# Kernel optimization log

Hardware: AMD Instinct MI355X
Metric: run time of the kernel (lower is better)

Reference implementation:

```python
import jax, jax.numpy as jnp
import numpy as np

N = 50000   # nodes
E = 512000  # edges
D = 64      # embedding_dim
L = 4       # num_layers
ATOM_DIMS = np.array([119, 5, 12, 12, 10, 6, 6, 2, 2])  # OGB atom feature vocab sizes
BOND_DIMS = np.array([5, 6, 2])                          # OGB bond feature vocab sizes


def _ln(x, g, b, eps=1e-5):
    m = x.mean(-1, keepdims=True)
    v = x.var(-1, keepdims=True)
    return (x - m) * jax.lax.rsqrt(v + eps) * g + b


def setup_inputs() -> dict:
    key = jax.random.key(0)
    ks = jax.random.split(key, 12)
    s = 0.05
    x = jax.random.randint(ks[0], (N, 9), 0, jnp.asarray(ATOM_DIMS)[None, :])
    edge_attr = jax.random.randint(ks[1], (E, 3), 0, jnp.asarray(BOND_DIMS)[None, :])
    edge_index = jax.random.randint(ks[2], (2, E), 0, N)
    # padded embedding tables: [n_feats, max_vocab, D]
    atom_emb = jax.random.normal(ks[3], (9, 119, D), jnp.float32) * s
    bond_emb = jax.random.normal(ks[4], (3, 6, D), jnp.float32) * s
    eps = jnp.zeros((L,), jnp.float32)  # GIN eps, init 0
    W1 = jax.random.normal(ks[5], (L, D, 2 * D), jnp.float32) * s
    b1 = jnp.zeros((L, 2 * D), jnp.float32)
    W2 = jax.random.normal(ks[6], (L, 2 * D, D), jnp.float32) * s
    b2 = jnp.zeros((L, D), jnp.float32)
    ln_g = jnp.ones((L, D), jnp.float32)
    ln_b = jnp.zeros((L, D), jnp.float32)
    Wu1 = jax.random.normal(ks[7], (L, 3 * D, 3 * D), jnp.float32) * s
    bu1 = jnp.zeros((L, 3 * D), jnp.float32)
    ug = jnp.ones((L, 3 * D), jnp.float32)
    ub = jnp.zeros((L, 3 * D), jnp.float32)
    Wu2 = jax.random.normal(ks[8], (L, 3 * D, D), jnp.float32) * s
    bu2 = jnp.zeros((L, D), jnp.float32)
    return dict(x=x, edge_attr=edge_attr, edge_index=edge_index,
                atom_emb=atom_emb, bond_emb=bond_emb, eps=eps,
                W1=W1, b1=b1, W2=W2, b2=b2, ln_g=ln_g, ln_b=ln_b,
                Wu1=Wu1, bu1=bu1, ug=ug, ub=ub, Wu2=Wu2, bu2=bu2)


def reference(x, edge_attr, edge_index, atom_emb, bond_emb, eps,
              W1, b1, W2, b2, ln_g, ln_b, Wu1, bu1, ug, ub, Wu2, bu2):
    # Atom/Bond encoders: sum of per-column categorical embeddings
    node = atom_emb[jnp.arange(9)[None, :], x].sum(axis=1)       # [N, D]
    edge = bond_emb[jnp.arange(3)[None, :], edge_attr].sum(axis=1)  # [E, D]
    src, dst = edge_index[0], edge_index[1]
    for l in range(L):
        # MyGINConv (GINE): aggregate relu(x_src + e) at dst, mlp((1+eps)x + agg)
        msg = jax.nn.relu(node[src] + edge)                      # [E, D]
        agg = jax.ops.segment_sum(msg, dst, num_segments=N)      # [N, D]
        h = (1.0 + eps[l]) * node + agg
        h = jax.nn.relu(h @ W1[l] + b1[l]) @ W2[l] + b2[l]       # conv MLP
        h = _ln(h, ln_g[l], ln_b[l])                             # batch_norms[l] (LayerNorm)
        node = jax.nn.relu(h) + node                             # dropout=identity (eval) + residual
        # SparseEdgeUpdateLayer (residual=True)
        cat = jnp.concatenate([node[src], node[dst], edge], axis=-1)  # [E, 3D]
        m = _ln(cat @ Wu1[l] + bu1[l], ug[l], ub[l])
        edge = jax.nn.relu(m) @ Wu2[l] + bu2[l] + edge
    return node, edge
```

## Files before the change

### kernel.cpp

```cpp
#include <hip/hip_runtime.h>
#include <hip/hip_bf16.h>


#define GIN_N 50000
#define GIN_E 512000

typedef __attribute__((ext_vector_type(8))) short short8;
typedef __attribute__((ext_vector_type(4))) float f32x4;
typedef unsigned short u16;

__device__ __forceinline__ u16 bf16r(float x) {
    unsigned u = __builtin_bit_cast(unsigned, x);
    u += 0x7fffu + ((u >> 16) & 1u);
    return (u16)(u >> 16);
}
__device__ __forceinline__ float bf16f(u16 h) {
    unsigned u = ((unsigned)h) << 16;
    return __builtin_bit_cast(float, u);
}

__global__ __launch_bounds__(256) void zero_f32(float* __restrict__ p, int n) {
    int i = blockIdx.x * 256 + threadIdx.x;
    if (i < n) p[i] = 0.f;
}

__global__ __launch_bounds__(256) void atom_encode(const int* __restrict__ x,
        const float* __restrict__ emb, float* __restrict__ node, int N) {
    int idx = blockIdx.x * 256 + threadIdx.x;
    int n = idx >> 6, lane = idx & 63;
    if (n >= N) return;
    float s = 0.f;
#pragma unroll
    for (int f = 0; f < 9; ++f) {
        int v = x[n * 9 + f];
        s += emb[(f * 119 + v) * 64 + lane];
    }
    node[(size_t)n * 64 + lane] = s;
}

__global__ __launch_bounds__(256) void bond_encode_scatter(
        const int* __restrict__ ea, const float* __restrict__ emb,
        u16* __restrict__ edgeB, const int* __restrict__ src,
        const int* __restrict__ dst, const float* __restrict__ node,
        float* __restrict__ agg, int E) {
    int idx = blockIdx.x * 256 + threadIdx.x;
    int e = idx >> 6, lane = idx & 63;
    if (e >= E) return;
    float s = 0.f;
#pragma unroll
    for (int f = 0; f < 3; ++f) {
        int v = ea[e * 3 + f];
        s += emb[(f * 6 + v) * 64 + lane];
    }
    edgeB[(size_t)e * 64 + lane] = bf16r(s);
    int si = src[e], di = dst[e];
    float msg = fmaxf(node[(size_t)si * 64 + lane] + s, 0.f);
    unsafeAtomicAdd(&agg[(size_t)di * 64 + lane], msg);
}

__global__ __launch_bounds__(256) void pack_b1(const float* __restrict__ W,
        u16* __restrict__ out, int K, int Nc, int F) {
    int tid = blockIdx.x * 256 + threadIdx.x;
    int lane = tid & 63;
    int frag = (tid >> 6) % F;
    int layer = tid / (F * 64);
    int tpr = Nc / 16;
    int ks = frag / tpr, tt = frag % tpr;
    int k0 = ks * 32 + ((lane >> 4) << 3);
    int col = tt * 16 + (lane & 15);
    const float* w = W + (size_t)layer * K * Nc;
    u16* o = out + ((size_t)layer * F + frag) * 512 + (size_t)lane * 8;
#pragma unroll
    for (int j = 0; j < 8; ++j) o[j] = bf16r(w[(size_t)(k0 + j) * Nc + col]);
}
__global__ __launch_bounds__(256) void pack_b2(const float* __restrict__ W,
        u16* __restrict__ out, int K, int Nc, int F) {
    int tid = blockIdx.x * 256 + threadIdx.x;
    int lane = tid & 63;
    int frag = (tid >> 6) % F;
    int layer = tid / (F * 64);
    int tpr = Nc / 16;
    int ks = frag / tpr, tt = frag % tpr;
    int k0 = ks * 32 + ((lane >> 4) << 3);
    int col = tt * 16 + (lane & 15);
    const float* w = W + (size_t)layer * K * Nc;
    u16* o = out + ((size_t)layer * F + frag) * 1024 + (size_t)lane * 8;
#pragma unroll
    for (int j = 0; j < 8; ++j) {
        float v = w[(size_t)(k0 + j) * Nc + col];
        u16 hi = bf16r(v);
        o[j] = hi;
        o[512 + j] = bf16r(v - bf16f(hi));
    }
}

__global__ __launch_bounds__(256, 2) void node_mlp(
        float* __restrict__ node, u16* __restrict__ nodeB,
        float* __restrict__ agg,
        const float* __restrict__ epsArr, int l,
        const u16* __restrict__ pw1, const u16* __restrict__ pw2,
        const float* __restrict__ b1, const float* __restrict__ b2,
        const float* __restrict__ lng, const float* __restrict__ lnb, int N) {
    __shared__ u16 xH[64][72], xL[64][72];
    __shared__ u16 hH[64][136], hL[64][136];
    __shared__ float pS[4][64], pS2[4][64], lnM[64], lnR[64];
    const int t = threadIdx.x, w = t >> 6, lane = t & 63;
    const int g = lane >> 4, c0 = lane & 15;
    const float epf = 1.f + epsArr[l];

#pragma unroll
    for (int i = 0; i < 16; ++i) {
        int r = w * 16 + i;
        int n = blockIdx.x * 64 + r;
        float x = 0.f;
        if (n < N) {
            size_t o = (size_t)n * 64 + lane;
            x = epf * node[o] + agg[o];
            agg[o] = 0.f;
        }
        u16 h = bf16r(x);
        xH[r][lane] = h;
        xL[r][lane] = bf16r(x - bf16f(h));
    }
    __syncthreads();

    f32x4 a1[4][2];
#pragma unroll
    for (int sp = 0; sp < 4; ++sp)
#pragma unroll
        for (int lt = 0; lt < 2; ++lt) a1[sp][lt] = (f32x4)0.f;
#pragma unroll
    for (int ks = 0; ks < 2; ++ks) {
        short8 aH[4], aL[4];
#pragma unroll
        for (int sp = 0; sp < 4; ++sp) {
            aH[sp] = *(const short8*)&xH[sp * 16 + c0][ks * 32 + g * 8];
            aL[sp] = *(const short8*)&xL[sp * 16 + c0][ks * 32 + g * 8];
        }
#pragma unroll
        for (int lt = 0; lt < 2; ++lt) {
            const u16* p = pw1 + (size_t)(ks * 8 + w * 2 + lt) * 1024 + (size_t)lane * 8;
            short8 bH = *(const short8*)p;
            short8 bL = *(const short8*)(p + 512);
#pragma unroll
            for (int sp = 0; sp < 4; ++sp) {
                a1[sp][lt] = __builtin_amdgcn_mfma_f32_16x16x32_bf16(aH[sp], bH, a1[sp][lt], 0, 0, 0);
                a1[sp][lt] = __builtin_amdgcn_mfma_f32_16x16x32_bf16(aH[sp], bL, a1[sp][lt], 0, 0, 0);
                a1[sp][lt] = __builtin_amdgcn_mfma_f32_16x16x32_bf16(aL[sp], bH, a1[sp][lt], 0, 0, 0);
            }
        }
    }
#pragma unroll
    for (int lt = 0; lt < 2; ++lt) {
        int col = w * 32 + lt * 16 + c0;
        float bias = b1[col];
#pragma unroll
        for (int sp = 0; sp < 4; ++sp)
#pragma unroll
            for (int rg = 0; rg < 4; ++rg) {
                int r = sp * 16 + g * 4 + rg;
                float v = fmaxf(a1[sp][lt][rg] + bias, 0.f);
                u16 h = bf16r(v);
                hH[r][col] = h;
                hL[r][col] = bf16r(v - bf16f(h));
            }
    }
    __syncthreads();

    f32x4 a2[4];
#pragma unroll
    for (int sp = 0; sp < 4; ++sp) a2[sp] = (f32x4)0.f;
#pragma unroll
    for (int ks = 0; ks < 4; ++ks) {
        const u16* p = pw2 + (size_t)(ks * 4 + w) * 1024 + (size_t)lane * 8;
        short8 bH = *(const short8*)p;
        short8 bL = *(const short8*)(p + 512);
#pragma unroll
        for (int sp = 0; sp < 4; ++sp) {
            short8 aH = *(const short8*)&hH[sp * 16 + c0][ks * 32 + g * 8];
            short8 aL = *(const short8*)&hL[sp * 16 + c0][ks * 32 + g * 8];
            a2[sp] = __builtin_amdgcn_mfma_f32_16x16x32_bf16(aH, bH, a2[sp], 0, 0, 0);
            a2[sp] = __builtin_amdgcn_mfma_f32_16x16x32_bf16(aH, bL, a2[sp], 0, 0, 0);
            a2[sp] = __builtin_amdgcn_mfma_f32_16x16x32_bf16(aL, bH, a2[sp], 0, 0, 0);
        }
    }
    float bias2 = b2[w * 16 + c0];
    float s1v[4][4], s2v[4][4];
#pragma unroll
    for (int sp = 0; sp < 4; ++sp)
#pragma unroll
        for (int rg = 0; rg < 4; ++rg) {
            float v = a2[sp][rg] + bias2;
            a2[sp][rg] = v;
            s1v[sp][rg] = v;
            s2v[sp][rg] = v * v;
        }
#pragma unroll
    for (int off = 1; off < 16; off <<= 1)
#pragma unroll
        for (int sp = 0; sp < 4; ++sp)
#pragma unroll
            for (int rg = 0; rg < 4; ++rg) {
                s1v[sp][rg] += __shfl_xor(s1v[sp][rg], off);
                s2v[sp][rg] += __shfl_xor(s2v[sp][rg], off);
            }
    if (c0 == 0) {
#pragma unroll
        for (int sp = 0; sp < 4; ++sp)
#pragma unroll
            for (int rg = 0; rg < 4; ++rg) {
                int r = sp * 16 + g * 4 + rg;
                pS[w][r] = s1v[sp][rg];
                pS2[w][r] = s2v[sp][rg];
            }
    }
    __syncthreads();
    if (t < 64) {
        float a = pS[0][t] + pS[1][t] + pS[2][t] + pS[3][t];
        float b = pS2[0][t] + pS2[1][t] + pS2[2][t] + pS2[3][t];
        float mean = a * (1.f / 64.f);
        float var = b * (1.f / 64.f) - mean * mean;
        lnM[t] = mean;
        lnR[t] = rsqrtf(var + 1e-5f);
    }
    __syncthreads();

    int col = w * 16 + c0;
    float gg = lng[col], bc = lnb[col];
#pragma unroll
    for (int sp = 0; sp < 4; ++sp)
#pragma unroll
        for (int rg = 0; rg < 4; ++rg) {
            int r = sp * 16 + g * 4 + rg;
            int n = blockIdx.x * 64 + r;
            if (n < N) {
                size_t o = (size_t)n * 64 + col;
                float y = (a2[sp][rg] - lnM[r]) * lnR[r] * gg + bc;
                float out = fmaxf(y, 0.f) + node[o];
                node[o] = out;
                nodeB[o] = bf16r(out);
            }
        }
}

template <bool SCATTER>
__global__ __launch_bounds__(256, 4) void edge_update_v6(
        const int* __restrict__ src, const int* __restrict__ dst,
        const float* __restrict__ node, const u16* __restrict__ nodeB,
        u16* __restrict__ edgeB, float* __restrict__ edgeF,
        float* __restrict__ agg,
        const u16* __restrict__ pb1, const u16* __restrict__ pb2,
        const float* __restrict__ bu1, const float* __restrict__ ug,
        const float* __restrict__ ub, const float* __restrict__ bu2) {
    __shared__ u16 cat[64][202];
    __shared__ u16 eold[64][66];
    __shared__ float pS[4][64], pS2[4][64];
    __shared__ float lnM[64], lnR[64];
    const int t = threadIdx.x, w = t >> 6, lane = t & 63;
    const int g = lane >> 4, c0 = lane & 15;
    const long eB = (long)blockIdx.x * 64;

#pragma unroll
    for (int i = 0; i < 16; ++i) {
        int r = w * 16 + i;
        long ge = eB + r;
        int s = src[ge], d = dst[ge];
        cat[r][lane]       = nodeB[(size_t)s * 64 + lane];
        cat[r][64 + lane]  = nodeB[(size_t)d * 64 + lane];
        u16 ev = edgeB[(size_t)ge * 64 + lane];
        cat[r][128 + lane] = ev;
        eold[r][lane] = ev;
    }
    __syncthreads();

    f32x4 acc[4][3];
#pragma unroll
    for (int sp = 0; sp < 4; ++sp)
#pragma unroll
        for (int lt = 0; lt < 3; ++lt) acc[sp][lt] = (f32x4)0.f;
#pragma unroll
    for (int ks = 0; ks < 6; ++ks) {
        short8 a[4];
#pragma unroll
        for (int sp = 0; sp < 4; ++sp)
            a[sp] = *(const short8*)&cat[sp * 16 + c0][ks * 32 + g * 8];
#pragma unroll
        for (int lt = 0; lt < 3; ++lt) {
            const u16* p = pb1 + (size_t)(ks * 12 + w * 3 + lt) * 512 + (size_t)lane * 8;
            short8 b = *(const short8*)p;
#pragma unroll
            for (int sp = 0; sp < 4; ++sp)
                acc[sp][lt] = __builtin_amdgcn_mfma_f32_16x16x32_bf16(a[sp], b, acc[sp][lt], 0, 0, 0);
        }
    }

    float bs[3];
#pragma unroll
    for (int lt = 0; lt < 3; ++lt) bs[lt] = bu1[w * 48 + lt * 16 + c0];
    float s1v[4][4], s2v[4][4];
#pragma unroll
    for (int sp = 0; sp < 4; ++sp)
#pragma unroll
        for (int rg = 0; rg < 4; ++rg) { s1v[sp][rg] = 0.f; s2v[sp][rg] = 0.f; }
#pragma unroll
    for (int sp = 0; sp < 4; ++sp)
#pragma unroll
        for (int lt = 0; lt < 3; ++lt)
#pragma unroll
            for (int rg = 0; rg < 4; ++rg) {
                float v = acc[sp][lt][rg] + bs[lt];
                acc[sp][lt][rg] = v;
                s1v[sp][rg] += v;
                s2v[sp][rg] += v * v;
            }
#pragma unroll
    for (int off = 1; off < 16; off <<= 1)
#pragma unroll
        for (int sp = 0; sp < 4; ++sp)
#pragma unroll
            for (int rg = 0; rg < 4; ++rg) {
                s1v[sp][rg] += __shfl_xor(s1v[sp][rg], off);
                s2v[sp][rg] += __shfl_xor(s2v[sp][rg], off);
            }
    if (c0 == 0) {
#pragma unroll
        for (int sp = 0; sp < 4; ++sp)
#pragma unroll
            for (int rg = 0; rg < 4; ++rg) {
                int r = sp * 16 + g * 4 + rg;
                pS[w][r] = s1v[sp][rg];
                pS2[w][r] = s2v[sp][rg];
            }
    }
    __syncthreads();
    if (t < 64) {
        float a = pS[0][t] + pS[1][t] + pS[2][t] + pS[3][t];
        float b = pS2[0][t] + pS2[1][t] + pS2[2][t] + pS2[3][t];
        float mean = a * (1.f / 192.f);
        float var = b * (1.f / 192.f) - mean * mean;
        lnM[t] = mean;
        lnR[t] = rsqrtf(var + 1e-5f);
    }
    __syncthreads();

#pragma unroll
    for (int lt = 0; lt < 3; ++lt) {
        int col = w * 48 + lt * 16 + c0;
        float gg = ug[col], bb = ub[col];
#pragma unroll
        for (int sp = 0; sp < 4; ++sp)
#pragma unroll
            for (int rg = 0; rg < 4; ++rg) {
                int r = sp * 16 + g * 4 + rg;
                float v = (acc[sp][lt][rg] - lnM[r]) * lnR[r] * gg + bb;
                cat[r][col] = bf16r(fmaxf(v, 0.f));
            }
    }
    __syncthreads();

    f32x4 a2[4];
#pragma unroll
    for (int sp = 0; sp < 4; ++sp) a2[sp] = (f32x4)0.f;
#pragma unroll
    for (int ks = 0; ks < 6; ++ks) {
        const u16* p = pb2 + (size_t)(ks * 4 + w) * 512 + (size_t)lane * 8;
        short8 b = *(const short8*)p;
#pragma unroll
        for (int sp = 0; sp < 4; ++sp) {
            short8 a = *(const short8*)&cat[sp * 16 + c0][ks * 32 + g * 8];
            a2[sp] = __builtin_amdgcn_mfma_f32_16x16x32_bf16(a, b, a2[sp], 0, 0, 0);
        }
    }

    const int col = w * 16 + c0;
    const float bb2 = bu2[col];
#pragma unroll
    for (int sp = 0; sp < 4; ++sp)
#pragma unroll
        for (int rg = 0; rg < 4; ++rg) {
            int r = sp * 16 + g * 4 + rg;
            long ge = eB + r;
            float eNew = a2[sp][rg] + bb2 + bf16f(eold[r][col]);
            if (SCATTER) {
                edgeB[(size_t)ge * 64 + col] = bf16r(eNew);
                int s2 = src[ge], d2 = dst[ge];
                float msg = fmaxf(node[(size_t)s2 * 64 + col] + eNew, 0.f);
                unsafeAtomicAdd(&agg[(size_t)d2 * 64 + col], msg);
            } else {
                edgeF[(size_t)ge * 64 + col] = eNew;
            }
        }
}

extern "C" void kernel_launch(void* const* d_in, const int* in_sizes, int n_in,
                              void* d_out, int out_size, void* d_ws, size_t ws_size,
                              hipStream_t stream) {
    const int*   x         = (const int*)d_in[0];
    const int*   edge_attr = (const int*)d_in[1];
    const int*   edge_index= (const int*)d_in[2];
    const float* atom_emb  = (const float*)d_in[3];
    const float* bond_emb  = (const float*)d_in[4];
    const float* eps       = (const float*)d_in[5];
    const float* W1        = (const float*)d_in[6];
    const float* b1        = (const float*)d_in[7];
    const float* W2        = (const float*)d_in[8];
    const float* b2        = (const float*)d_in[9];
    const float* ln_g      = (const float*)d_in[10];
    const float* ln_b      = (const float*)d_in[11];
    const float* Wu1       = (const float*)d_in[12];
    const float* bu1       = (const float*)d_in[13];
    const float* ug        = (const float*)d_in[14];
    const float* ub        = (const float*)d_in[15];
    const float* Wu2       = (const float*)d_in[16];
    const float* bu2       = (const float*)d_in[17];

    const int N = GIN_N, E = GIN_E;
    const int* src = edge_index;
    const int* dst = edge_index + E;

    float* node  = (float*)d_out;
    float* edgeF = (float*)d_out + (size_t)N * 64;

    char* ws = (char*)d_ws;
    float* agg   = (float*)ws;  ws += (size_t)N * 64 * 4;
    u16*   nodeB = (u16*)ws;    ws += (size_t)N * 64 * 2;
    u16*   edgeB = (u16*)ws;    ws += (size_t)E * 64 * 2;
    u16* pb1     = (u16*)ws;    ws += (size_t)4 * 72 * 512 * 2;
    u16* pb2     = (u16*)ws;    ws += (size_t)4 * 24 * 512 * 2;
    u16* pw1     = (u16*)ws;    ws += (size_t)4 * 16 * 1024 * 2;
    u16* pw2     = (u16*)ws;    ws += (size_t)4 * 16 * 1024 * 2;

    pack_b1<<<(4 * 72 * 64) / 256, 256, 0, stream>>>(Wu1, pb1, 192, 192, 72);
    pack_b1<<<(4 * 24 * 64) / 256, 256, 0, stream>>>(Wu2, pb2, 192, 64, 24);
    pack_b2<<<(4 * 16 * 64) / 256, 256, 0, stream>>>(W1, pw1, 64, 128, 16);
    pack_b2<<<(4 * 16 * 64) / 256, 256, 0, stream>>>(W2, pw2, 128, 64, 16);

    atom_encode<<<(N * 64 + 255) / 256, 256, 0, stream>>>(x, atom_emb, node, N);
    zero_f32<<<(N * 64) / 256, 256, 0, stream>>>(agg, N * 64);
    bond_encode_scatter<<<(E * 64) / 256, 256, 0, stream>>>(edge_attr, bond_emb,
        edgeB, src, dst, node, agg, E);

    const int nodeBlocks = (N + 63) / 64;
    for (int l = 0; l < 4; ++l) {
        node_mlp<<<nodeBlocks, 256, 0, stream>>>(node, nodeB, agg, eps, l,
            pw1 + (size_t)l * 16 * 1024, pw2 + (size_t)l * 16 * 1024,
            b1 + (size_t)l * 128, b2 + (size_t)l * 64,
            ln_g + (size_t)l * 64, ln_b + (size_t)l * 64, N);
        if (l < 3)
            edge_update_v6<true><<<E / 64, 256, 0, stream>>>(src, dst, node, nodeB,
                edgeB, edgeF, agg,
                pb1 + (size_t)l * 72 * 512, pb2 + (size_t)l * 24 * 512,
                bu1 + (size_t)l * 192,
                ug + (size_t)l * 192, ub + (size_t)l * 192,
                bu2 + (size_t)l * 64);
        else
            edge_update_v6<false><<<E / 64, 256, 0, stream>>>(src, dst, node, nodeB,
                edgeB, edgeF, agg,
                pb1 + (size_t)l * 72 * 512, pb2 + (size_t)l * 24 * 512,
                bu1 + (size_t)l * 192,
                ug + (size_t)l * 192, ub + (size_t)l * 192,
                bu2 + (size_t)l * 64);
    }
}
```

Before: 912.7 us.

## Sort edges by destination via CSR and pre-reduce scatter atomics in shared memory

Builds a destination-sorted edge permutation each call (histogram, single-block scan, atomic fill) and processes edges in sorted order. Edge messages are staged in shared memory and summed over runs of equal destination, so one atomic is issued per run instead of per edge. The final edge output is written back through the permutation. Block indices are also remapped with an 8-way interleave to spread tiles. This adds several preprocessing kernels, including a serial single-block scan, and makes the final edge writes scattered.

```diff
diff --git a/kernel.cpp b/kernel.cpp
--- a/kernel.cpp
+++ b/kernel.cpp
@@ -22,6 +22,10 @@
 __global__ __launch_bounds__(256) void zero_f32(float* __restrict__ p, int n) {
     int i = blockIdx.x * 256 + threadIdx.x;
     if (i < n) p[i] = 0.f;
+}
+__global__ __launch_bounds__(256) void zero_i32(int* __restrict__ p, int n) {
+    int i = blockIdx.x * 256 + threadIdx.x;
+    if (i < n) p[i] = 0;
 }
 
 __global__ __launch_bounds__(256) void atom_encode(const int* __restrict__ x,
@@ -38,22 +42,73 @@
     node[(size_t)n * 64 + lane] = s;
 }
 
+__global__ __launch_bounds__(256) void csr_hist(const int* __restrict__ dst,
+                                                int* __restrict__ deg, int E) {
+    int e = blockIdx.x * 256 + threadIdx.x;
+    if (e < E) atomicAdd(&deg[dst[e]], 1);
+}
+__global__ __launch_bounds__(256) void csr_scan(const int* __restrict__ deg,
+                                                int* __restrict__ cursor, int N) {
+    __shared__ int ps[256];
+    const int t = threadIdx.x;
+    const int chunk = (N + 255) / 256;
+    const int base = t * chunk;
+    int s = 0;
+    for (int i = 0; i < chunk; ++i) {
+        int idx = base + i;
+        if (idx < N) s += deg[idx];
+    }
+    ps[t] = s;
+    __syncthreads();
+    for (int off = 1; off < 256; off <<= 1) {
+        int v = (t >= off) ? ps[t - off] : 0;
+        __syncthreads();
+        ps[t] += v;
+        __syncthreads();
+    }
+    int run = ps[t] - s;
+    for (int i = 0; i < chunk; ++i) {
+        int idx = base + i;
+        if (idx < N) { cursor[idx] = run; run += deg[idx]; }
+    }
+}
+__global__ __launch_bounds__(256) void csr_fill(const int* __restrict__ dst,
+        int* __restrict__ cursor, int* __restrict__ perm, int E) {
+    int e = blockIdx.x * 256 + threadIdx.x;
+    if (e < E) {
+        int d = dst[e];
+        int pos = atomicAdd(&cursor[d], 1);
+        perm[pos] = e;
+    }
+}
+__global__ __launch_bounds__(256) void permute_ei(const int* __restrict__ src,
+        const int* __restrict__ dst, const int* __restrict__ perm,
+        int* __restrict__ srcS, int* __restrict__ dstS, int E) {
+    int i = blockIdx.x * 256 + threadIdx.x;
+    if (i < E) {
+        int pe = perm[i];
+        srcS[i] = src[pe];
+        dstS[i] = dst[pe];
+    }
+}
+
 __global__ __launch_bounds__(256) void bond_encode_scatter(
         const int* __restrict__ ea, const float* __restrict__ emb,
-        u16* __restrict__ edgeB, const int* __restrict__ src,
-        const int* __restrict__ dst, const float* __restrict__ node,
-        float* __restrict__ agg, int E) {
+        u16* __restrict__ edgeB, const int* __restrict__ perm,
+        const int* __restrict__ srcS, const int* __restrict__ dstS,
+        const float* __restrict__ node, float* __restrict__ agg, int E) {
     int idx = blockIdx.x * 256 + threadIdx.x;
     int e = idx >> 6, lane = idx & 63;
     if (e >= E) return;
+    int pe = perm[e];
     float s = 0.f;
 #pragma unroll
     for (int f = 0; f < 3; ++f) {
-        int v = ea[e * 3 + f];
+        int v = ea[pe * 3 + f];
         s += emb[(f * 6 + v) * 64 + lane];
     }
     edgeB[(size_t)e * 64 + lane] = bf16r(s);
-    int si = src[e], di = dst[e];
+    int si = srcS[e], di = dstS[e];
     float msg = fmaxf(node[(size_t)si * 64 + lane] + s, 0.f);
     unsafeAtomicAdd(&agg[(size_t)di * 64 + lane], msg);
 }
@@ -244,8 +299,9 @@
 }
 
 template <bool SCATTER>
-__global__ __launch_bounds__(256, 4) void edge_update_v6(
+__global__ __launch_bounds__(256, 4) void edge_update_v7(
         const int* __restrict__ src, const int* __restrict__ dst,
+        const int* __restrict__ perm,
         const float* __restrict__ node, const u16* __restrict__ nodeB,
         u16* __restrict__ edgeB, float* __restrict__ edgeF,
         float* __restrict__ agg,
@@ -256,10 +312,13 @@
     __shared__ u16 eold[64][66];
     __shared__ float pS[4][64], pS2[4][64];
     __shared__ float lnM[64], lnR[64];
+    __shared__ int dstL[64], srcL[64];
     const int t = threadIdx.x, w = t >> 6, lane = t & 63;
     const int g = lane >> 4, c0 = lane & 15;
-    const long eB = (long)blockIdx.x * 64;
-
+    const int tile = (blockIdx.x & 7) * (gridDim.x >> 3) + (blockIdx.x >> 3);
+    const long eB = (long)tile * 64;
+
+    if (t < 64) { dstL[t] = dst[eB + t]; srcL[t] = src[eB + t]; }
 #pragma unroll
     for (int i = 0; i < 16; ++i) {
         int r = w * 16 + i;
@@ -371,7 +430,9 @@
             a2[sp] = __builtin_amdgcn_mfma_f32_16x16x32_bf16(a, b, a2[sp], 0, 0, 0);
         }
     }
-
+    __syncthreads();
+
+    float* msgF = (float*)&cat[0][0];
     const int col = w * 16 + c0;
     const float bb2 = bu2[col];
 #pragma unroll
@@ -383,13 +444,28 @@
             float eNew = a2[sp][rg] + bb2 + bf16f(eold[r][col]);
             if (SCATTER) {
                 edgeB[(size_t)ge * 64 + col] = bf16r(eNew);
-                int s2 = src[ge], d2 = dst[ge];
-                float msg = fmaxf(node[(size_t)s2 * 64 + col] + eNew, 0.f);
-                unsafeAtomicAdd(&agg[(size_t)d2 * 64 + col], msg);
+                float msg = fmaxf(node[(size_t)srcL[r] * 64 + col] + eNew, 0.f);
+                msgF[r * 66 + col] = msg;
             } else {
-                edgeF[(size_t)ge * 64 + col] = eNew;
-            }
-        }
+                edgeF[(size_t)perm[ge] * 64 + col] = eNew;
+            }
+        }
+
+    if (SCATTER) {
+        __syncthreads();
+        const int colR = t & 63;
+        const int h = t >> 6;
+        float accm = 0.f;
+#pragma unroll 1
+        for (int r = h * 16; r < h * 16 + 16; ++r) {
+            accm += msgF[r * 66 + colR];
+            bool flush = (r == h * 16 + 15) || (dstL[r + 1] != dstL[r]);
+            if (flush) {
+                unsafeAtomicAdd(&agg[(size_t)dstL[r] * 64 + colR], accm);
+                accm = 0.f;
+            }
+        }
+    }
 }
 
 extern "C" void kernel_launch(void* const* d_in, const int* in_sizes, int n_in,
@@ -425,6 +501,11 @@
     float* agg   = (float*)ws;  ws += (size_t)N * 64 * 4;
     u16*   nodeB = (u16*)ws;    ws += (size_t)N * 64 * 2;
     u16*   edgeB = (u16*)ws;    ws += (size_t)E * 64 * 2;
+    int*   perm  = (int*)ws;    ws += (size_t)E * 4;
+    int*   srcS  = (int*)ws;    ws += (size_t)E * 4;
+    int*   dstS  = (int*)ws;    ws += (size_t)E * 4;
+    int*   deg   = (int*)ws;    ws += (size_t)N * 4;
+    int*   cursor= (int*)ws;    ws += (size_t)(N + 1) * 4;
     u16* pb1     = (u16*)ws;    ws += (size_t)4 * 72 * 512 * 2;
     u16* pb2     = (u16*)ws;    ws += (size_t)4 * 24 * 512 * 2;
     u16* pw1     = (u16*)ws;    ws += (size_t)4 * 16 * 1024 * 2;
@@ -435,10 +516,16 @@
     pack_b2<<<(4 * 16 * 64) / 256, 256, 0, stream>>>(W1, pw1, 64, 128, 16);
     pack_b2<<<(4 * 16 * 64) / 256, 256, 0, stream>>>(W2, pw2, 128, 64, 16);
 
+    zero_i32<<<(N + 255) / 256, 256, 0, stream>>>(deg, N);
+    csr_hist<<<E / 256, 256, 0, stream>>>(dst, deg, E);
+    csr_scan<<<1, 256, 0, stream>>>(deg, cursor, N);
+    csr_fill<<<E / 256, 256, 0, stream>>>(dst, cursor, perm, E);
+    permute_ei<<<E / 256, 256, 0, stream>>>(src, dst, perm, srcS, dstS, E);
+
     atom_encode<<<(N * 64 + 255) / 256, 256, 0, stream>>>(x, atom_emb, node, N);
     zero_f32<<<(N * 64) / 256, 256, 0, stream>>>(agg, N * 64);
     bond_encode_scatter<<<(E * 64) / 256, 256, 0, stream>>>(edge_attr, bond_emb,
-        edgeB, src, dst, node, agg, E);
+        edgeB, perm, srcS, dstS, node, agg, E);
 
     const int nodeBlocks = (N + 63) / 64;
     for (int l = 0; l < 4; ++l) {
@@ -447,15 +534,15 @@
             b1 + (size_t)l * 128, b2 + (size_t)l * 64,
             ln_g + (size_t)l * 64, ln_b + (size_t)l * 64, N);
         if (l < 3)
-            edge_update_v6<true><<<E / 64, 256, 0, stream>>>(src, dst, node, nodeB,
-                edgeB, edgeF, agg,
+            edge_update_v7<true><<<E / 64, 256, 0, stream>>>(srcS, dstS, perm,
+                node, nodeB, edgeB, edgeF, agg,
                 pb1 + (size_t)l * 72 * 512, pb2 + (size_t)l * 24 * 512,
                 bu1 + (size_t)l * 192,
                 ug + (size_t)l * 192, ub + (size_t)l * 192,
                 bu2 + (size_t)l * 64);
         else
-            edge_update_v6<false><<<E / 64, 256, 0, stream>>>(src, dst, node, nodeB,
-                edgeB, edgeF, agg,
+            edge_update_v7<false><<<E / 64, 256, 0, stream>>>(srcS, dstS, perm,
+                node, nodeB, edgeB, edgeF, agg,
                 pb1 + (size_t)l * 72 * 512, pb2 + (size_t)l * 24 * 512,
                 bu1 + (size_t)l * 192,
                 ug + (size_t)l * 192, ub + (size_t)l * 192,
```

Result: slower. 1.016 ms (+11.4%).
